# Kernel optimization log

Hardware: AMD Instinct MI355X
Metric: run time of the kernel (lower is better)

The kernel has to match this reference:

```python
import jax, jax.numpy as jnp
import numpy as np

N, K, D = 65536, 16, 64  # points, neighbors, d_out
EPS = 1e-5


def setup_inputs() -> dict:
    key = jax.random.key(0)
    ks = jax.random.split(key, 10)
    s = lambda fan: 1.0 / np.sqrt(fan)
    return {
        "p": jax.random.normal(ks[0], (N, K, 3), jnp.float32),
        "x": jax.random.normal(ks[1], (N, K, D), jnp.float32),
        # BiMLP: Conv1d(10, 2D, 1) -> BN -> ReLU -> Conv1d(2D, D, 1)
        "w1": jax.random.normal(ks[2], (10, 2 * D), jnp.float32) * s(10),
        "b1": jnp.zeros((2 * D,), jnp.float32),
        "g1": jnp.ones((2 * D,), jnp.float32),
        "be1": jnp.zeros((2 * D,), jnp.float32),
        "w2": jax.random.normal(ks[3], (2 * D, D), jnp.float32) * s(2 * D),
        "b2": jnp.zeros((D,), jnp.float32),
        # score_fn: Linear(2D, 2D, bias=False)
        "ws": jax.random.normal(ks[4], (2 * D, 2 * D), jnp.float32) * s(2 * D),
        # mlp_out: Linear(2D, D) -> BN -> ReLU
        "wo": jax.random.normal(ks[5], (2 * D, D), jnp.float32) * s(2 * D),
        "bo": jnp.zeros((D,), jnp.float32),
        "g2": jnp.ones((D,), jnp.float32),
        "be2": jnp.zeros((D,), jnp.float32),
    }


def reference(p, x, w1, b1, g1, be1, w2, b2, ws, wo, bo, g2, be2):
    # p: [N,K,3] neighbor coords (index 0 is the center), x: [N,K,D]
    center = p[:, :1, :]                                   # [N,1,3]
    diff = center - p                                      # [N,K,3]
    dist = jnp.sqrt(jnp.sum(diff * diff, axis=2, keepdims=True))  # [N,K,1]
    concat = jnp.concatenate(
        [jnp.broadcast_to(center, p.shape), p, diff, dist], axis=-1)  # [N,K,10]

    # 1x1 conv == per-point linear over channel dim
    h = jnp.einsum('nkc,cd->nkd', concat, w1) + b1          # [N,K,2D]
    # BatchNorm1d over (N,K) per channel (training-mode batch stats)
    mu = jnp.mean(h, axis=(0, 1))
    var = jnp.var(h, axis=(0, 1))
    h = (h - mu) * jax.lax.rsqrt(var + EPS) * g1 + be1
    h = jax.nn.relu(h)
    p_c = jnp.einsum('nkd,de->nke', h, w2) + b2             # [N,K,D]

    p_x = jnp.concatenate([p_c, x], axis=-1)                # [N,K,2D]
    # attention scores: linear (no bias) then softmax over neighbor dim (-2)
    scores = jax.nn.softmax(jnp.einsum('nkd,de->nke', p_x, ws), axis=-2)
    feat = jnp.sum(scores * p_x, axis=1)                    # [N,2D]

    out = feat @ wo + bo                                    # [N,D]
    mu2 = jnp.mean(out, axis=0)
    var2 = jnp.var(out, axis=0)
    out = (out - mu2) * jax.lax.rsqrt(var2 + EPS) * g2 + be2
    return jax.nn.relu(out)
```

## Files before the change

kernel.cpp:

```cpp
#include <hip/hip_runtime.h>
#include <math.h>

#define NPTS 65536
#define EPSV 1e-5f
#define B1G  256
#define B3G  1024

#define OFF_P1  0
#define OFF_S1  (B1G*65)
#define OFF_P2  (OFF_S1+256)
#define OFF_S2  (OFF_P2+B3G*128)
#define OFF_PRE (OFF_S2+128)

typedef unsigned int u32;
typedef short v8s __attribute__((ext_vector_type(8)));
typedef float v4f __attribute__((ext_vector_type(4)));

union F8 { v8s v; u32 u[4]; unsigned short s[8]; };

__device__ __forceinline__ u32 f2bf(float f){
  u32 u = __float_as_uint(f);
  return (u + 0x7fffu + ((u>>16)&1u)) >> 16;
}
__device__ __forceinline__ float bf2f(unsigned short s){ return __uint_as_float(((u32)s)<<16); }
__device__ __forceinline__ u32 packbf(float a, float b){
  u32 r; asm("v_cvt_pk_bf16_f32 %0, %1, %2" : "=v"(r) : "v"(a), "v"(b)); return r;
}
__device__ __forceinline__ float rcpf(float x){
  float r; asm("v_rcp_f32 %0, %1" : "=v"(r) : "v"(x)); return r;
}
__device__ __forceinline__ int chmap(int p){ return 32*(p>>5) + ((p&31)>>1) + 16*(p&1); }

__global__ __launch_bounds__(256) void k1_stats(const float* __restrict__ p, float* __restrict__ part1){
  int tid = blockIdx.x*256 + threadIdx.x;
  float M[55]; float s[10];
  #pragma unroll
  for(int i=0;i<55;i++) M[i]=0.f;
  #pragma unroll
  for(int i=0;i<10;i++) s[i]=0.f;
  for(int it=0; it<16; ++it){
    int r = it*65536 + tid;
    int n = r >> 4;
    int kk = r & 15;
    const float* pn = p + (size_t)n*48;
    float cx=pn[0], cy=pn[1], cz=pn[2];
    float ax=pn[kk*3+0], ay=pn[kk*3+1], az=pn[kk*3+2];
    float dx=cx-ax, dy=cy-ay, dz=cz-az;
    float dd = sqrtf(dx*dx+dy*dy+dz*dz);
    float c[10]={cx,cy,cz,ax,ay,az,dx,dy,dz,dd};
    #pragma unroll
    for(int i=0;i<10;i++) s[i]+=c[i];
    int idx=0;
    #pragma unroll
    for(int i=0;i<10;i++){
      #pragma unroll
      for(int j=i;j<10;j++){
        M[idx] = fmaf(c[i],c[j],M[idx]);
        idx++;
      }
    }
  }
  #pragma unroll
  for(int i=0;i<10;i++){
    for(int off=32; off>0; off>>=1) s[i] += __shfl_down(s[i], off, 64);
  }
  #pragma unroll
  for(int i=0;i<55;i++){
    for(int off=32; off>0; off>>=1) M[i] += __shfl_down(M[i], off, 64);
  }
  __shared__ float sm[4][65];
  int lane = threadIdx.x & 63, w = threadIdx.x >> 6;
  if(lane==0){
    #pragma unroll
    for(int i=0;i<10;i++) sm[w][i]=s[i];
    #pragma unroll
    for(int i=0;i<55;i++) sm[w][10+i]=M[i];
  }
  __syncthreads();
  if(threadIdx.x<65){
    float v = sm[0][threadIdx.x]+sm[1][threadIdx.x]+sm[2][threadIdx.x]+sm[3][threadIdx.x];
    part1[blockIdx.x*65 + threadIdx.x] = v;
  }
}

__device__ __forceinline__ int tri_idx(int i,int j){
  int a = i<j? i : j;
  int b = i<j? j : i;
  return 10*a - (a*(a-1))/2 + (b-a);
}
__global__ __launch_bounds__(256) void k2_fin(const float* __restrict__ part1, const float* __restrict__ w1,
                       const float* __restrict__ g1, const float* __restrict__ be1,
                       float* __restrict__ stats1){
  __shared__ float P[4][65];
  __shared__ float S[65];
  int t = threadIdx.x;
  for(int idx=t; idx<260; idx+=256){
    int seg = idx/65, v = idx - seg*65;
    float a=0.f;
    for(int b=seg; b<B1G; b+=4) a += part1[b*65+v];
    P[seg][v]=a;
  }
  __syncthreads();
  if(t<65) S[t] = P[0][t]+P[1][t]+P[2][t]+P[3][t];
  __syncthreads();
  if(t<128){
    float wc[10];
    #pragma unroll
    for(int c=0;c<10;c++) wc[c]=w1[c*128+t];
    float md=0.f;
    #pragma unroll
    for(int c=0;c<10;c++) md += S[c]*wc[c];
    const float invR = 1.0f/(float)(NPTS*16);
    md *= invR;
    float q=0.f;
    #pragma unroll
    for(int i=0;i<10;i++){
      float ti=0.f;
      #pragma unroll
      for(int j=0;j<10;j++) ti += S[10+tri_idx(i,j)]*wc[j];
      q = fmaf(ti, wc[i], q);
    }
    q *= invR;
    float var = q - md*md;
    float sc = g1[t]*rsqrtf(var+EPSV);
    float sh = be1[t] - md*sc;
    stats1[t]=sc;
    stats1[128+t]=sh;
  }
}

__global__ __launch_bounds__(256,4) void k3_main(
    const float* __restrict__ p, const float* __restrict__ x,
    const float* __restrict__ w2, const float* __restrict__ b2,
    const float* __restrict__ wsm, const float* __restrict__ wo,
    const float* __restrict__ w1, const float* __restrict__ stats1,
    float* __restrict__ pre, float* __restrict__ part2)
{
  __shared__ unsigned short s_h [4][16][136];
  __shared__ unsigned short s_px[4][16][136];
  __shared__ unsigned short s_ft[16][136];

  const int tid  = threadIdx.x;
  const int w    = tid>>6;
  const int lane = tid&63;
  const int q    = lane>>4;
  const int c    = lane&15;

  v8s Bw1[2], Bw2[4], Bws[2][4], Bwo[4];
  #pragma unroll
  for(int t=0;t<2;t++){
    F8 f;
    #pragma unroll
    for(int j=0;j<8;j++){
      int k = q*8+j;
      f.s[j] = (unsigned short)(k<10 ? f2bf(w1[k*128 + 32*w + 16*t + c]) : 0);
    }
    Bw1[t]=f.v;
  }
  #pragma unroll
  for(int kk=0;kk<4;kk++){
    F8 f;
    #pragma unroll
    for(int j=0;j<8;j++) f.s[j]=(unsigned short)f2bf(w2[chmap(kk*32+q*8+j)*64 + 16*w + c]);
    Bw2[kk]=f.v;
  }
  #pragma unroll
  for(int t=0;t<2;t++){
    #pragma unroll
    for(int kk=0;kk<4;kk++){
      F8 f;
      #pragma unroll
      for(int j=0;j<8;j++) f.s[j]=(unsigned short)f2bf(wsm[(kk*32+q*8+j)*128 + 32*w + 16*t + c]);
      Bws[t][kk]=f.v;
    }
  }
  #pragma unroll
  for(int kk=0;kk<4;kk++){
    F8 f;
    #pragma unroll
    for(int j=0;j<8;j++) f.s[j]=(unsigned short)f2bf(wo[chmap(kk*32+q*8+j)*64 + 16*w + c]);
    Bwo[kk]=f.v;
  }
  const float sc1a = stats1[32*w+c],    sh1a = stats1[128+32*w+c];
  const float sc1b = stats1[32*w+16+c], sh1b = stats1[128+32*w+16+c];
  const float b2v  = b2[16*w+c];

  float a_s=0.f, a_q=0.f;
  const int base0 = blockIdx.x*64;

  unsigned short *xd0, *xd1, *xd2, *xd3;
  {
    int f;
    f = tid;       xd0 = &s_px[f>>8][(f&255)>>4][64+4*(f&15)];
    f = tid+256;   xd1 = &s_px[f>>8][(f&255)>>4][64+4*(f&15)];
    f = tid+512;   xd2 = &s_px[f>>8][(f&255)>>4][64+4*(f&15)];
    f = tid+768;   xd3 = &s_px[f>>8][(f&255)>>4][64+4*(f&15)];
  }
  float4 xr0, xr1, xr2, xr3;
  {
    const float4* xg = (const float4*)(x + (size_t)base0*1024);
    xr0 = xg[tid]; xr1 = xg[tid+256]; xr2 = xg[tid+512]; xr3 = xg[tid+768];
  }

  for(int r=0;r<16;++r){
    const int base = base0 + 4*r;

    *(uint2*)xd0 = make_uint2(packbf(xr0.x,xr0.y), packbf(xr0.z,xr0.w));
    *(uint2*)xd1 = make_uint2(packbf(xr1.x,xr1.y), packbf(xr1.z,xr1.w));
    *(uint2*)xd2 = make_uint2(packbf(xr2.x,xr2.y), packbf(xr2.z,xr2.w));
    *(uint2*)xd3 = make_uint2(packbf(xr3.x,xr3.y), packbf(xr3.z,xr3.w));
    if(r<15){
      const float4* xg = (const float4*)(x + (size_t)(base+4)*1024);
      xr0 = xg[tid]; xr1 = xg[tid+256]; xr2 = xg[tid+512]; xr3 = xg[tid+768];
    }

    #pragma unroll
    for(int n0=0;n0<4;n0++){
      const float* pn = p + (size_t)(base+n0)*48;
      float cx=pn[0], cy=pn[1], cz=pn[2];
      float ax=pn[3*c], ay=pn[3*c+1], az=pn[3*c+2];
      float dx=cx-ax, dy=cy-ay, dz=cz-az;
      float dd=sqrtf(dx*dx+dy*dy+dz*dz);
      u32 pk01=packbf(cx,cy), pk23=packbf(cz,ax), pk45=packbf(ay,az),
          pk67=packbf(dx,dy), pk89=packbf(dz,dd);
      F8 fa;
      fa.u[0] = q==0 ? pk01 : (q==1 ? pk89 : 0u);
      fa.u[1] = q==0 ? pk23 : 0u;
      fa.u[2] = q==0 ? pk45 : 0u;
      fa.u[3] = q==0 ? pk67 : 0u;
      v4f z={0.f,0.f,0.f,0.f};
      v4f d0 = __builtin_amdgcn_mfma_f32_16x16x32_bf16(fa.v, Bw1[0], z, 0,0,0);
      v4f d1 = __builtin_amdgcn_mfma_f32_16x16x32_bf16(fa.v, Bw1[1], z, 0,0,0);
      #pragma unroll
      for(int i=0;i<4;i++){
        float v0 = fmaxf(0.f, fmaf(d0[i], sc1a, sh1a));
        float v1 = fmaxf(0.f, fmaf(d1[i], sc1b, sh1b));
        *(u32*)&s_h[n0][4*q+i][32*w+2*c] = packbf(v0, v1);
      }
    }
    __syncthreads();

    #pragma unroll
    for(int n0=0;n0<4;n0++){
      const v8s* Ar = (const v8s*)&s_h[n0][c][0];
      v4f acc={0.f,0.f,0.f,0.f};
      #pragma unroll
      for(int kk=0;kk<4;kk++)
        acc = __builtin_amdgcn_mfma_f32_16x16x32_bf16(Ar[kk*4+q], Bw2[kk], acc, 0,0,0);
      #pragma unroll
      for(int i=0;i<4;i+=2){
        u32 pk = packbf(acc[i]+b2v, acc[i+1]+b2v);
        s_px[n0][4*q+i][16*w+c]   = (unsigned short)pk;
        s_px[n0][4*q+i+1][16*w+c] = (unsigned short)(pk>>16);
      }
    }
    __syncthreads();

    #pragma unroll
    for(int n0=0;n0<4;n0++){
      const v8s* Ar = (const v8s*)&s_px[n0][c][0];
      v4f l0={0.f,0.f,0.f,0.f}, l1={0.f,0.f,0.f,0.f};
      #pragma unroll
      for(int kk=0;kk<4;kk++){
        v8s a = Ar[kk*4+q];
        l0 = __builtin_amdgcn_mfma_f32_16x16x32_bf16(a, Bws[0][kk], l0, 0,0,0);
        l1 = __builtin_amdgcn_mfma_f32_16x16x32_bf16(a, Bws[1][kk], l1, 0,0,0);
      }
      float se0=0.f, se1=0.f, fe0=0.f, fe1=0.f;
      #pragma unroll
      for(int i=0;i<4;i++){
        int pt = 4*q+i;
        float p0 = bf2f(s_px[n0][pt][32*w+c]);
        float p1 = bf2f(s_px[n0][pt][32*w+16+c]);
        float E0 = __expf(l0[i]);
        float E1 = __expf(l1[i]);
        se0 += E0; se1 += E1;
        fe0 = fmaf(E0, p0, fe0);
        fe1 = fmaf(E1, p1, fe1);
      }
      se0 += __shfl_xor(se0,16); se0 += __shfl_xor(se0,32);
      se1 += __shfl_xor(se1,16); se1 += __shfl_xor(se1,32);
      fe0 += __shfl_xor(fe0,16); fe0 += __shfl_xor(fe0,32);
      fe1 += __shfl_xor(fe1,16); fe1 += __shfl_xor(fe1,32);
      if(q==0){
        const int slot = (r&3)*4 + n0;
        *(u32*)&s_ft[slot][32*w+2*c] = packbf(fe0*rcpf(se0), fe1*rcpf(se1));
      }
    }
    __syncthreads();

    if((r&3)==3){
      const v8s* Ar = (const v8s*)&s_ft[c][0];
      v4f o={0.f,0.f,0.f,0.f};
      #pragma unroll
      for(int kk=0;kk<4;kk++)
        o = __builtin_amdgcn_mfma_f32_16x16x32_bf16(Ar[kk*4+q], Bwo[kk], o, 0,0,0);
      const int nb16 = base0 + (r>>2)*16;
      #pragma unroll
      for(int i=0;i<4;i++){
        float val = o[i];
        pre[(size_t)(nb16 + 4*q + i)*64 + 16*w + c] = val;
        a_s += val;
        a_q = fmaf(val,val,a_q);
      }
    }
  }

  a_s += __shfl_xor(a_s, 16, 64); a_s += __shfl_xor(a_s, 32, 64);
  a_q += __shfl_xor(a_q, 16, 64); a_q += __shfl_xor(a_q, 32, 64);
  if(q==0){
    part2[blockIdx.x*128 + 16*w + c]      = a_s;
    part2[blockIdx.x*128 + 64 + 16*w + c] = a_q;
  }
}

__global__ __launch_bounds__(512) void k4_fin(const float* __restrict__ part2, const float* __restrict__ g2,
                       const float* __restrict__ be2, float* __restrict__ stats2){
  __shared__ float sm[8][128];
  int t = threadIdx.x;
  int d = t & 63, seg = t >> 6;
  float s=0.f, qq=0.f;
  for(int i=0;i<B3G/8;i++){
    int b = seg + 8*i;
    s  += part2[b*128+d];
    qq += part2[b*128+64+d];
  }
  sm[seg][d]    = s;
  sm[seg][64+d] = qq;
  __syncthreads();
  if(t<64){
    float S=0.f, Q=0.f;
    #pragma unroll
    for(int k=0;k<8;k++){ S += sm[k][t]; Q += sm[k][64+t]; }
    float mu  = S/(float)NPTS;
    float var = Q/(float)NPTS - mu*mu;
    float sc = g2[t]*rsqrtf(var+EPSV);
    float sh = be2[t] - mu*sc;
    stats2[t]=sc;
    stats2[64+t]=sh;
  }
}

__global__ __launch_bounds__(256) void k5_apply(const float* __restrict__ pre,
                                                const float* __restrict__ stats2,
                                                float* __restrict__ out){
  int i = blockIdx.x*256 + threadIdx.x;
  float4 v = ((const float4*)pre)[i];
  int d4 = i & 15;
  float4 sc = ((const float4*)stats2)[d4];
  float4 sh = ((const float4*)(stats2+64))[d4];
  float4 o;
  o.x = fmaxf(0.f, fmaf(v.x,sc.x,sh.x));
  o.y = fmaxf(0.f, fmaf(v.y,sc.y,sh.y));
  o.z = fmaxf(0.f, fmaf(v.z,sc.z,sh.z));
  o.w = fmaxf(0.f, fmaf(v.w,sc.w,sh.w));
  ((float4*)out)[i] = o;
}

extern "C" void kernel_launch(void* const* d_in, const int* in_sizes, int n_in,
                              void* d_out, int out_size, void* d_ws, size_t ws_size,
                              hipStream_t stream){
  (void)in_sizes; (void)n_in; (void)out_size; (void)ws_size;
  const float* p   = (const float*)d_in[0];
  const float* x   = (const float*)d_in[1];
  const float* w1  = (const float*)d_in[2];
  const float* g1  = (const float*)d_in[4];
  const float* be1 = (const float*)d_in[5];
  const float* w2  = (const float*)d_in[6];
  const float* b2  = (const float*)d_in[7];
  const float* wsm = (const float*)d_in[8];
  const float* wo  = (const float*)d_in[9];
  const float* g2  = (const float*)d_in[11];
  const float* be2 = (const float*)d_in[12];

  float* wsf    = (float*)d_ws;
  float* part1  = wsf + OFF_P1;
  float* stats1 = wsf + OFF_S1;
  float* part2  = wsf + OFF_P2;
  float* stats2 = wsf + OFF_S2;
  float* pre    = wsf + OFF_PRE;
  float* out    = (float*)d_out;

  k1_stats<<<B1G,256,0,stream>>>(p, part1);
  k2_fin  <<<1,256,0,stream>>>(part1, w1, g1, be1, stats1);
  k3_main <<<B3G,256,0,stream>>>(p,x,w2,b2,wsm,wo,w1,stats1,pre,part2);
  k4_fin  <<<1,512,0,stream>>>(part2,g2,be2,stats2);
  k5_apply<<<4096,256,0,stream>>>(pre,stats2,out);
}
```

Before: 506.2 us.

## Fold w2 into score weights to skip pc staging and one barrier

Precomputes W2·Ws[0:64] and b2·Ws in a new small kernel, so attention logits for the pc half come straight from the hidden activations, alongside pc itself. This removes the LDS round trip for p_c and one __syncthreads per iteration, and shrinks the LDS staging buffer to x only. Other changes: p neighbor coords are prefetched one step ahead with the center fetched via a shuffle, wo fragments are reloaded only when needed to cut register pressure, and k4 uses more threads. The trade-offs are an extra kernel launch, more MFMAs per point, and the folded weights are rounded to bf16 as a product, which slightly changes numerics.

Result: slower. 725.3 us (+43.3%).

```diff
diff --git a/kernel.cpp b/kernel.cpp
--- a/kernel.cpp
+++ b/kernel.cpp
@@ -30,8 +30,9 @@
   float r; asm("v_rcp_f32 %0, %1" : "=v"(r) : "v"(x)); return r;
 }
 __device__ __forceinline__ int chmap(int p){ return 32*(p>>5) + ((p&31)>>1) + 16*(p&1); }
-
-__global__ __launch_bounds__(256) void k1_stats(const float* __restrict__ p, float* __restrict__ part1){
+__device__ __forceinline__ int chmap2(int p){ return 16*(p>>5) + ((p&31)>>1) + 64*(p&1); }
+
+__global__ __launch_bounds__(256,1) void k1_stats(const float* __restrict__ p, float* __restrict__ part1){
   int tid = blockIdx.x*256 + threadIdx.x;
   float M[55]; float s[10];
   #pragma unroll
@@ -129,15 +130,30 @@
   }
 }
 
+__global__ __launch_bounds__(256) void k2c_w2s(const float* __restrict__ w2, const float* __restrict__ wsm,
+                        const float* __restrict__ b2, float* __restrict__ w2s){
+  int gid = blockIdx.x*256 + threadIdx.x;
+  int k = gid >> 7, e = gid & 127;
+  float a = 0.f;
+  for(int d=0; d<64; d++) a = fmaf(w2[k*64+d], wsm[d*128+e], a);
+  w2s[k*128+e] = a;
+  if(gid < 128){
+    float cbv = 0.f;
+    for(int d=0; d<64; d++) cbv = fmaf(b2[d], wsm[d*128+gid], cbv);
+    w2s[16384+gid] = cbv;
+  }
+}
+
 __global__ __launch_bounds__(256,4) void k3_main(
     const float* __restrict__ p, const float* __restrict__ x,
     const float* __restrict__ w2, const float* __restrict__ b2,
     const float* __restrict__ wsm, const float* __restrict__ wo,
     const float* __restrict__ w1, const float* __restrict__ stats1,
+    const float* __restrict__ w2s,
     float* __restrict__ pre, float* __restrict__ part2)
 {
   __shared__ unsigned short s_h [4][16][136];
-  __shared__ unsigned short s_px[4][16][136];
+  __shared__ unsigned short s_x [4][16][72];
   __shared__ unsigned short s_ft[16][136];
 
   const int tid  = threadIdx.x;
@@ -146,7 +162,7 @@
   const int q    = lane>>4;
   const int c    = lane&15;
 
-  v8s Bw1[2], Bw2[4], Bws[2][4], Bwo[4];
+  v8s Bw1[2], Bw2[4], BSlo[4], BShi[4], Bbl[2], Bbh[2];
   #pragma unroll
   for(int t=0;t<2;t++){
     F8 f;
@@ -159,31 +175,32 @@
   }
   #pragma unroll
   for(int kk=0;kk<4;kk++){
-    F8 f;
-    #pragma unroll
-    for(int j=0;j<8;j++) f.s[j]=(unsigned short)f2bf(w2[chmap(kk*32+q*8+j)*64 + 16*w + c]);
-    Bw2[kk]=f.v;
-  }
-  #pragma unroll
-  for(int t=0;t<2;t++){
-    #pragma unroll
-    for(int kk=0;kk<4;kk++){
-      F8 f;
-      #pragma unroll
-      for(int j=0;j<8;j++) f.s[j]=(unsigned short)f2bf(wsm[(kk*32+q*8+j)*128 + 32*w + 16*t + c]);
-      Bws[t][kk]=f.v;
-    }
-  }
-  #pragma unroll
-  for(int kk=0;kk<4;kk++){
-    F8 f;
-    #pragma unroll
-    for(int j=0;j<8;j++) f.s[j]=(unsigned short)f2bf(wo[chmap(kk*32+q*8+j)*64 + 16*w + c]);
-    Bwo[kk]=f.v;
+    F8 f, g, h2;
+    #pragma unroll
+    for(int j=0;j<8;j++){
+      int row = chmap(kk*32+q*8+j);
+      f.s[j]  = (unsigned short)f2bf(w2 [row*64  + 16*w + c]);
+      g.s[j]  = (unsigned short)f2bf(w2s[row*128 + 16*w + c]);
+      h2.s[j] = (unsigned short)f2bf(w2s[row*128 + 64 + 16*w + c]);
+    }
+    Bw2[kk]=f.v; BSlo[kk]=g.v; BShi[kk]=h2.v;
+  }
+  #pragma unroll
+  for(int kk=0;kk<2;kk++){
+    F8 f, g;
+    #pragma unroll
+    for(int j=0;j<8;j++){
+      int row = 64 + kk*32+q*8+j;
+      f.s[j] = (unsigned short)f2bf(wsm[row*128 + 16*w + c]);
+      g.s[j] = (unsigned short)f2bf(wsm[row*128 + 64 + 16*w + c]);
+    }
+    Bbl[kk]=f.v; Bbh[kk]=g.v;
   }
   const float sc1a = stats1[32*w+c],    sh1a = stats1[128+32*w+c];
   const float sc1b = stats1[32*w+16+c], sh1b = stats1[128+32*w+16+c];
   const float b2v  = b2[16*w+c];
+  const float cb_lo = w2s[16384 + 16*w+c];
+  const float cb_hi = w2s[16384 + 64+16*w+c];
 
   float a_s=0.f, a_q=0.f;
   const int base0 = blockIdx.x*64;
@@ -191,34 +208,40 @@
   unsigned short *xd0, *xd1, *xd2, *xd3;
   {
     int f;
-    f = tid;       xd0 = &s_px[f>>8][(f&255)>>4][64+4*(f&15)];
-    f = tid+256;   xd1 = &s_px[f>>8][(f&255)>>4][64+4*(f&15)];
-    f = tid+512;   xd2 = &s_px[f>>8][(f&255)>>4][64+4*(f&15)];
-    f = tid+768;   xd3 = &s_px[f>>8][(f&255)>>4][64+4*(f&15)];
+    f = tid;       xd0 = &s_x[f>>8][(f&255)>>4][4*(f&15)];
+    f = tid+256;   xd1 = &s_x[f>>8][(f&255)>>4][4*(f&15)];
+    f = tid+512;   xd2 = &s_x[f>>8][(f&255)>>4][4*(f&15)];
+    f = tid+768;   xd3 = &s_x[f>>8][(f&255)>>4][4*(f&15)];
   }
   float4 xr0, xr1, xr2, xr3;
+  float pax0,pay0,paz0, pax1,pay1,paz1, pax2,pay2,paz2, pax3,pay3,paz3;
   {
     const float4* xg = (const float4*)(x + (size_t)base0*1024);
     xr0 = xg[tid]; xr1 = xg[tid+256]; xr2 = xg[tid+512]; xr3 = xg[tid+768];
+    const float* pn0 = p + (size_t)(base0+0)*48;
+    const float* pn1 = p + (size_t)(base0+1)*48;
+    const float* pn2 = p + (size_t)(base0+2)*48;
+    const float* pn3 = p + (size_t)(base0+3)*48;
+    pax0=pn0[3*c]; pay0=pn0[3*c+1]; paz0=pn0[3*c+2];
+    pax1=pn1[3*c]; pay1=pn1[3*c+1]; paz1=pn1[3*c+2];
+    pax2=pn2[3*c]; pay2=pn2[3*c+1]; paz2=pn2[3*c+2];
+    pax3=pn3[3*c]; pay3=pn3[3*c+1]; paz3=pn3[3*c+2];
   }
 
   for(int r=0;r<16;++r){
-    const int base = base0 + 4*r;
-
     *(uint2*)xd0 = make_uint2(packbf(xr0.x,xr0.y), packbf(xr0.z,xr0.w));
     *(uint2*)xd1 = make_uint2(packbf(xr1.x,xr1.y), packbf(xr1.z,xr1.w));
     *(uint2*)xd2 = make_uint2(packbf(xr2.x,xr2.y), packbf(xr2.z,xr2.w));
     *(uint2*)xd3 = make_uint2(packbf(xr3.x,xr3.y), packbf(xr3.z,xr3.w));
-    if(r<15){
-      const float4* xg = (const float4*)(x + (size_t)(base+4)*1024);
-      xr0 = xg[tid]; xr1 = xg[tid+256]; xr2 = xg[tid+512]; xr3 = xg[tid+768];
-    }
 
     #pragma unroll
     for(int n0=0;n0<4;n0++){
-      const float* pn = p + (size_t)(base+n0)*48;
-      float cx=pn[0], cy=pn[1], cz=pn[2];
-      float ax=pn[3*c], ay=pn[3*c+1], az=pn[3*c+2];
+      float ax = n0==0?pax0 : n0==1?pax1 : n0==2?pax2 : pax3;
+      float ay = n0==0?pay0 : n0==1?pay1 : n0==2?pay2 : pay3;
+      float az = n0==0?paz0 : n0==1?paz1 : n0==2?paz2 : paz3;
+      float cx = __shfl(ax, 0, 64);
+      float cy = __shfl(ay, 0, 64);
+      float cz = __shfl(az, 0, 64);
       float dx=cx-ax, dy=cy-ay, dz=cz-az;
       float dd=sqrtf(dx*dx+dy*dy+dz*dz);
       u32 pk01=packbf(cx,cy), pk23=packbf(cz,ax), pk45=packbf(ay,az),
@@ -238,58 +261,70 @@
         *(u32*)&s_h[n0][4*q+i][32*w+2*c] = packbf(v0, v1);
       }
     }
+
+    if(r<15){
+      const int nbase = base0 + 4*r + 4;
+      const float4* xg = (const float4*)(x + (size_t)nbase*1024);
+      xr0 = xg[tid]; xr1 = xg[tid+256]; xr2 = xg[tid+512]; xr3 = xg[tid+768];
+      const float* pn0 = p + (size_t)(nbase+0)*48;
+      const float* pn1 = p + (size_t)(nbase+1)*48;
+      const float* pn2 = p + (size_t)(nbase+2)*48;
+      const float* pn3 = p + (size_t)(nbase+3)*48;
+      pax0=pn0[3*c]; pay0=pn0[3*c+1]; paz0=pn0[3*c+2];
+      pax1=pn1[3*c]; pay1=pn1[3*c+1]; paz1=pn1[3*c+2];
+      pax2=pn2[3*c]; pay2=pn2[3*c+1]; paz2=pn2[3*c+2];
+      pax3=pn3[3*c]; pay3=pn3[3*c+1]; paz3=pn3[3*c+2];
+    }
     __syncthreads();
 
     #pragma unroll
     for(int n0=0;n0<4;n0++){
-      const v8s* Ar = (const v8s*)&s_h[n0][c][0];
-      v4f acc={0.f,0.f,0.f,0.f};
-      #pragma unroll
-      for(int kk=0;kk<4;kk++)
-        acc = __builtin_amdgcn_mfma_f32_16x16x32_bf16(Ar[kk*4+q], Bw2[kk], acc, 0,0,0);
-      #pragma unroll
-      for(int i=0;i<4;i+=2){
-        u32 pk = packbf(acc[i]+b2v, acc[i+1]+b2v);
-        s_px[n0][4*q+i][16*w+c]   = (unsigned short)pk;
-        s_px[n0][4*q+i+1][16*w+c] = (unsigned short)(pk>>16);
-      }
-    }
-    __syncthreads();
-
-    #pragma unroll
-    for(int n0=0;n0<4;n0++){
-      const v8s* Ar = (const v8s*)&s_px[n0][c][0];
-      v4f l0={0.f,0.f,0.f,0.f}, l1={0.f,0.f,0.f,0.f};
+      const v8s* Ah = (const v8s*)&s_h[n0][c][0];
+      const v8s* Ax = (const v8s*)&s_x[n0][c][0];
+      v4f acc={0.f,0.f,0.f,0.f}, llo={0.f,0.f,0.f,0.f}, lhi={0.f,0.f,0.f,0.f};
       #pragma unroll
       for(int kk=0;kk<4;kk++){
-        v8s a = Ar[kk*4+q];
-        l0 = __builtin_amdgcn_mfma_f32_16x16x32_bf16(a, Bws[0][kk], l0, 0,0,0);
-        l1 = __builtin_amdgcn_mfma_f32_16x16x32_bf16(a, Bws[1][kk], l1, 0,0,0);
-      }
-      float se0=0.f, se1=0.f, fe0=0.f, fe1=0.f;
+        v8s a = Ah[kk*4+q];
+        acc = __builtin_amdgcn_mfma_f32_16x16x32_bf16(a, Bw2[kk],  acc, 0,0,0);
+        llo = __builtin_amdgcn_mfma_f32_16x16x32_bf16(a, BSlo[kk], llo, 0,0,0);
+        lhi = __builtin_amdgcn_mfma_f32_16x16x32_bf16(a, BShi[kk], lhi, 0,0,0);
+      }
+      #pragma unroll
+      for(int kk=0;kk<2;kk++){
+        v8s a = Ax[kk*4+q];
+        llo = __builtin_amdgcn_mfma_f32_16x16x32_bf16(a, Bbl[kk], llo, 0,0,0);
+        lhi = __builtin_amdgcn_mfma_f32_16x16x32_bf16(a, Bbh[kk], lhi, 0,0,0);
+      }
+      float se_lo=0.f, se_hi=0.f, fe_lo=0.f, fe_hi=0.f;
       #pragma unroll
       for(int i=0;i<4;i++){
-        int pt = 4*q+i;
-        float p0 = bf2f(s_px[n0][pt][32*w+c]);
-        float p1 = bf2f(s_px[n0][pt][32*w+16+c]);
-        float E0 = __expf(l0[i]);
-        float E1 = __expf(l1[i]);
-        se0 += E0; se1 += E1;
-        fe0 = fmaf(E0, p0, fe0);
-        fe1 = fmaf(E1, p1, fe1);
-      }
-      se0 += __shfl_xor(se0,16); se0 += __shfl_xor(se0,32);
-      se1 += __shfl_xor(se1,16); se1 += __shfl_xor(se1,32);
-      fe0 += __shfl_xor(fe0,16); fe0 += __shfl_xor(fe0,32);
-      fe1 += __shfl_xor(fe1,16); fe1 += __shfl_xor(fe1,32);
+        float pcv = acc[i] + b2v;
+        float xv  = bf2f(s_x[n0][4*q+i][16*w+c]);
+        float El = __expf(llo[i] + cb_lo);
+        float Eh = __expf(lhi[i] + cb_hi);
+        se_lo += El; fe_lo = fmaf(El, pcv, fe_lo);
+        se_hi += Eh; fe_hi = fmaf(Eh, xv,  fe_hi);
+      }
+      se_lo += __shfl_xor(se_lo,16); se_lo += __shfl_xor(se_lo,32);
+      se_hi += __shfl_xor(se_hi,16); se_hi += __shfl_xor(se_hi,32);
+      fe_lo += __shfl_xor(fe_lo,16); fe_lo += __shfl_xor(fe_lo,32);
+      fe_hi += __shfl_xor(fe_hi,16); fe_hi += __shfl_xor(fe_hi,32);
       if(q==0){
         const int slot = (r&3)*4 + n0;
-        *(u32*)&s_ft[slot][32*w+2*c] = packbf(fe0*rcpf(se0), fe1*rcpf(se1));
+        *(u32*)&s_ft[slot][32*w+2*c] = packbf(fe_lo*rcpf(se_lo), fe_hi*rcpf(se_hi));
       }
     }
     __syncthreads();
 
     if((r&3)==3){
+      v8s Bwo[4];
+      #pragma unroll
+      for(int kk=0;kk<4;kk++){
+        F8 f;
+        #pragma unroll
+        for(int j=0;j<8;j++) f.s[j]=(unsigned short)f2bf(wo[chmap2(kk*32+q*8+j)*64 + 16*w + c]);
+        Bwo[kk]=f.v;
+      }
       const v8s* Ar = (const v8s*)&s_ft[c][0];
       v4f o={0.f,0.f,0.f,0.f};
       #pragma unroll
@@ -314,14 +349,14 @@
   }
 }
 
-__global__ __launch_bounds__(512) void k4_fin(const float* __restrict__ part2, const float* __restrict__ g2,
+__global__ __launch_bounds__(1024) void k4_fin(const float* __restrict__ part2, const float* __restrict__ g2,
                        const float* __restrict__ be2, float* __restrict__ stats2){
-  __shared__ float sm[8][128];
+  __shared__ float sm[16][128];
   int t = threadIdx.x;
   int d = t & 63, seg = t >> 6;
   float s=0.f, qq=0.f;
-  for(int i=0;i<B3G/8;i++){
-    int b = seg + 8*i;
+  for(int i=0;i<B3G/16;i++){
+    int b = seg + 16*i;
     s  += part2[b*128+d];
     qq += part2[b*128+64+d];
   }
@@ -331,7 +366,7 @@
   if(t<64){
     float S=0.f, Q=0.f;
     #pragma unroll
-    for(int k=0;k<8;k++){ S += sm[k][t]; Q += sm[k][64+t]; }
+    for(int k=0;k<16;k++){ S += sm[k][t]; Q += sm[k][64+t]; }
     float mu  = S/(float)NPTS;
     float var = Q/(float)NPTS - mu*mu;
     float sc = g2[t]*rsqrtf(var+EPSV);
@@ -383,7 +418,8 @@
 
   k1_stats<<<B1G,256,0,stream>>>(p, part1);
   k2_fin  <<<1,256,0,stream>>>(part1, w1, g1, be1, stats1);
-  k3_main <<<B3G,256,0,stream>>>(p,x,w2,b2,wsm,wo,w1,stats1,pre,part2);
-  k4_fin  <<<1,512,0,stream>>>(part2,g2,be2,stats2);
+  k2c_w2s <<<64,256,0,stream>>>(w2, wsm, b2, part1);
+  k3_main <<<B3G,256,0,stream>>>(p,x,w2,b2,wsm,wo,w1,stats1,part1,pre,part2);
+  k4_fin  <<<1,1024,0,stream>>>(part2,g2,be2,stats2);
   k5_apply<<<4096,256,0,stream>>>(pre,stats2,out);
 }
```
